# Kernel tuning notes

Measured on AMD Instinct MI355X. Metric: run time of the kernel, lower is better.

Reference implementation:

```python
import jax, jax.numpy as jnp
import numpy as np

B = 65536
NQ = 8
NL = 3
FEAT = 64 * 3 * 3 + NQ  # 584


def _conv(x, w, b):
    # x: (B,C,H,W), w: (O,I,3,3), padding=1 -> SAME
    y = jax.lax.conv_general_dilated(
        x, w, window_strides=(1, 1), padding='SAME',
        dimension_numbers=('NCHW', 'OIHW', 'NCHW'))
    return y + b[None, :, None, None]


def _maxpool2(x):
    return jax.lax.reduce_window(
        x, -jnp.inf, jax.lax.max, (1, 1, 2, 2), (1, 1, 2, 2), 'VALID')


def _quantum_sim(x, qp):
    # x: (B,NQ); qp: (NL,NQ,3). Within a layer, qubit q depends only on its own
    # previous state (tanh term), so vectorize over qubits and scan over layers.
    x_next = jnp.roll(x, -1, axis=1)  # x[:, (q+1) % NQ]

    def step(q_state, rot):  # rot: (NQ,3)
        new = jnp.sin(rot[:, 0] * x) * jnp.cos(rot[:, 1] * x_next) \
              + jnp.tanh(rot[:, 2] * q_state)
        return new, None

    q0 = jnp.zeros_like(x)
    qf, _ = jax.lax.scan(step, q0, qp)
    return qf


def setup_inputs() -> dict:
    key = jax.random.key(0)
    ks = jax.random.split(key, 16)

    def w(k, shape, fan_in):
        lim = 1.0 / np.sqrt(fan_in)
        return jax.random.uniform(k, shape, jnp.float32, -lim, lim)

    return {
        'board_state': jax.random.normal(ks[0], (B, 3, 6, 6), jnp.float32),
        'target_positions': jax.random.randint(ks[1], (4, 2), 0, 6).astype(jnp.int64),
        'conv1_w': w(ks[2], (16, 3, 3, 3), 3 * 9), 'conv1_b': w(ks[3], (16,), 3 * 9),
        'conv2_w': w(ks[4], (32, 16, 3, 3), 16 * 9), 'conv2_b': w(ks[5], (32,), 16 * 9),
        'conv3_w': w(ks[6], (64, 32, 3, 3), 32 * 9), 'conv3_b': w(ks[7], (64,), 32 * 9),
        'quantum_params': jax.random.normal(ks[8], (NL, NQ, 3), jnp.float32),
        'pt_w1': w(ks[9], (FEAT, 128), FEAT), 'pt_b1': w(ks[9], (128,), FEAT),
        'pt_w2': w(ks[10], (128, 64), 128), 'pt_b2': w(ks[10], (64,), 128),
        'pt_w3': w(ks[11], (64, 2), 64), 'pt_b3': w(ks[11], (2,), 64),
        'cf_w1': w(ks[12], (FEAT, 64), FEAT), 'cf_b1': w(ks[12], (64,), FEAT),
        'cf_w2': w(ks[13], (64, 1), 64), 'cf_b2': w(ks[13], (1,), 64),
    }


def reference(board_state, target_positions,
              conv1_w, conv1_b, conv2_w, conv2_b, conv3_w, conv3_b,
              quantum_params,
              pt_w1, pt_b1, pt_w2, pt_b2, pt_w3, pt_b3,
              cf_w1, cf_b1, cf_w2, cf_b2):
    b = board_state.shape[0]
    h = jax.nn.relu(_conv(board_state, conv1_w, conv1_b))   # (B,16,6,6)
    h = jax.nn.relu(_conv(h, conv2_w, conv2_b))             # (B,32,6,6)
    h = _maxpool2(h)                                        # (B,32,3,3)
    h = jax.nn.relu(_conv(h, conv3_w, conv3_b))             # (B,64,3,3)
    conv_flat = h.reshape(b, -1)                            # (B,576)

    board_flat = board_state.reshape(b, -1)
    q_feat = _quantum_sim(board_flat[:, :NQ], quantum_params)  # (B,NQ)

    feats = jnp.concatenate([conv_flat, q_feat], axis=1)    # (B,584)

    # piece-type head (Dropout is identity in eval)
    t = jax.nn.relu(feats @ pt_w1 + pt_b1)
    t = jax.nn.relu(t @ pt_w2 + pt_b2)
    type_logits = t @ pt_w3 + pt_b3
    type_probs = jax.nn.softmax(type_logits, axis=1)        # (B,2)

    # confidence head
    c = jax.nn.relu(feats @ cf_w1 + cf_b1)
    confidence = jax.nn.sigmoid(c @ cf_w2 + cf_b2)          # (B,1)

    # target_positions never affect the math (pos_encoding unused in torch source);
    # the same probs/confidence are reported for every position.
    return jnp.concatenate([type_probs, confidence], axis=1)  # (B,3)
```

## Files before the change

### kernel.cpp

```cpp
#include <hip/hip_runtime.h>

typedef _Float16 h8 __attribute__((ext_vector_type(8)));
typedef _Float16 h4 __attribute__((ext_vector_type(4)));
typedef float f32x4 __attribute__((ext_vector_type(4)));

union HU { _Float16 h; unsigned short u; };
__device__ __forceinline__ unsigned short f2h(float f) { HU x; x.h = (_Float16)f; return x.u; }
__device__ __forceinline__ float h2f(unsigned short u) { HU x; x.u = u; return (float)x.h; }

#define MFMA16(a, b, c) __builtin_amdgcn_mfma_f32_16x16x32_f16((a), (b), (c), 0, 0, 0)

__global__ void k_prep(const float* __restrict__ w1, const float* __restrict__ w2,
                       const float* __restrict__ w3,
                       const float* __restrict__ ptw1, const float* __restrict__ cfw1,
                       const float* __restrict__ ptw2, const float* __restrict__ ptw3,
                       const float* __restrict__ cfw2,
                       unsigned short* __restrict__ w1f,
                       unsigned short* __restrict__ w2f,
                       unsigned short* __restrict__ w3f,
                       unsigned short* __restrict__ w1hd,
                       unsigned short* __restrict__ w2hd,
                       unsigned short* __restrict__ w3hd) {
    int gid = blockIdx.x * 256 + threadIdx.x;
    int gs = gridDim.x * 256;
    for (int e = gid; e < 1024; e += gs) {
        int f = e >> 9, lane = (e >> 3) & 63, j = e & 7;
        int k = ((lane >> 4) << 3) + j, oc = lane & 15;
        int r, within;
        if (f == 0) { r = k >> 4; within = k & 15; }
        else        { r = 2;      within = k; }
        int tx = within >> 2, ch = within & 3;
        float v = 0.f;
        if (tx < 3 && ch < 3) v = w1[oc * 27 + ch * 9 + r * 3 + tx];
        w1f[e] = f2h(v);
    }
    for (int e = gid; e < 9216; e += gs) {
        int j = e & 7, lane = (e >> 3) & 63, fo = e >> 9;
        int ot = fo & 1, t = fo >> 1;
        int k = ((lane >> 4) * 8) + j, oc = ot * 16 + (lane & 15);
        float v = (k < 16) ? w2[oc * 144 + k * 9 + t] : 0.f;
        w2f[e] = f2h(v);
    }
    for (int e = gid; e < 18432; e += gs) {
        int j = e & 7, lane = (e >> 3) & 63, fo = e >> 9;
        int oti = fo & 1, t = (fo >> 1) % 9, otp = (fo >> 1) / 9;
        int ic = ((lane >> 4) * 8) + j, oc = (otp * 2 + oti) * 16 + (lane & 15);
        w3f[e] = f2h(w3[oc * 288 + ic * 9 + t]);
    }
    for (int s = gid; s < 608 * 192; s += gs) {
        int k = s / 192, n = s - k * 192;
        float v = 0.f;
        if (k < 584) {
            int f = (k < 576) ? ((k & 63) * 9 + (k >> 6)) : k;
            v = (n < 128) ? ptw1[f * 128 + n] : cfw1[f * 64 + (n - 128)];
        }
        int kk = k >> 5, hi = (k & 31) >> 3, j = k & 7, nt = n >> 4;
        int e = (((kk * 12 + nt) << 6) | (hi << 4) | (n & 15)) << 3 | j;
        w1hd[e] = f2h(v);
    }
    for (int s = gid; s < 8192; s += gs) {
        int k = s >> 6, n = s & 63;
        float v = ptw2[k * 64 + n];
        int kk = k >> 5, hi = (k & 31) >> 3, j = k & 7, nt = n >> 4;
        int e = ((((kk << 2) | nt) << 6) | (hi << 4) | (n & 15)) << 3 | j;
        w2hd[e] = f2h(v);
    }
    for (int e = gid; e < 2048; e += gs) {
        int j = e & 7, lane = (e >> 3) & 63, kk = e >> 9;
        int k = kk * 32 + ((lane >> 4) * 8) + j, n = lane & 15;
        float v = 0.f;
        if (k < 64) { if (n < 2) v = ptw3[k * 2 + n]; }
        else        { if (n == 2) v = cfw2[k - 64]; }
        w3hd[e] = f2h(v);
    }
}

#define BDS4 260
#define BDH4 (16 * BDS4)
#define A1S 584
#define A2S 296
#define FTS 616
#define HSH 200
#define RA_OFF 19712
#define O_OFF 26112
#define LDSTOT 26368

template<int PP0, int PP1>
__device__ __forceinline__ void conv2_compute(
    const unsigned short* A1, const h8* W2r, float b2v0, float b2v1,
    int sA1, int q, float pooled[5][2][4])
{
    #pragma unroll
    for (int pi = 0; pi < PP1 - PP0; pi++) {
        const int pp = PP0 + pi;
        #pragma unroll
        for (int sub = 0; sub < 4; sub++) {
            const int y = (pp / 3) * 2 + (sub >> 1), x = (pp % 3) * 2 + (sub & 1);
            f32x4 acc0 = {0.f, 0.f, 0.f, 0.f}, acc1 = {0.f, 0.f, 0.f, 0.f};
            #pragma unroll
            for (int t = 0; t < 9; t++) {
                const int sy = y + t / 3 - 1, sx = x + t % 3 - 1;
                if (sy < 0 || sy >= 6 || sx < 0 || sx >= 6) continue;
                h8 a = *(const h8*)&A1[sA1 + (sy * 6 + sx) * 16 + (q & 1) * 8];
                acc0 = MFMA16(a, W2r[t * 2 + 0], acc0);
                acc1 = MFMA16(a, W2r[t * 2 + 1], acc1);
            }
            #pragma unroll
            for (int r = 0; r < 4; r++) {
                pooled[pi][0][r] = fmaxf(pooled[pi][0][r], acc0[r] + b2v0);
                pooled[pi][1][r] = fmaxf(pooled[pi][1][r], acc1[r] + b2v1);
            }
        }
    }
}

template<int PP0, int PP1>
__device__ __forceinline__ void conv2_store(
    unsigned short* A2, const float pooled[5][2][4], int q, int col)
{
    #pragma unroll
    for (int pi = 0; pi < PP1 - PP0; pi++)
        #pragma unroll
        for (int ot = 0; ot < 2; ot++)
            #pragma unroll
            for (int r = 0; r < 4; r++)
                A2[(q * 4 + r) * A2S + (PP0 + pi) * 32 + ot * 16 + col] =
                    f2h(pooled[pi][ot][r]);
}

__global__ __launch_bounds__(256, 3) void k_fused(
    const float* __restrict__ board,
    const float* __restrict__ b1, const float* __restrict__ b2,
    const float* __restrict__ b3, const float* __restrict__ qp,
    const unsigned short* __restrict__ w1f,
    const unsigned short* __restrict__ w2f,
    const unsigned short* __restrict__ w3f,
    const unsigned short* __restrict__ w1hd,
    const unsigned short* __restrict__ w2hd,
    const unsigned short* __restrict__ w3hd,
    const float* __restrict__ ptb1, const float* __restrict__ ptb2,
    const float* __restrict__ ptb3, const float* __restrict__ cfb1,
    const float* __restrict__ cfb2,
    float* __restrict__ out)
{
    __shared__ __align__(16) unsigned short LDSH[LDSTOT];
    const int tid = threadIdx.x, wid = tid >> 6, lane = tid & 63;
    const int g = wid >> 1, w2 = wid & 1;
    const int col = lane & 15, q = lane >> 4;
    const long long gg0 = (long long)blockIdx.x * 32;
    const f32x4 ZERO4 = {0.f, 0.f, 0.f, 0.f};

    unsigned short* A1 = LDSH + g * 9856;
    unsigned short* A2 = A1;
    unsigned short* Hb = LDSH + RA_OFF;
    float* O = (float*)(LDSH + O_OFF);

    for (int e = tid; e < BDH4 / 4; e += 256)
        ((unsigned long long*)(LDSH + RA_OFF))[e] = 0ULL;
    __syncthreads();

    float qv[2];
    h8 w1r0 = ((const h8*)w1f)[lane];
    h8 w1r1 = ((const h8*)w1f)[64 + lane];
    float b1v = b1[col];
    #pragma unroll
    for (int gi = 0; gi < 2; gi++) {
        for (int e = tid; e < 16 * 108; e += 256) {
            int ss = e / 108, r2 = e % 108, ch = r2 / 36, p = r2 % 36;
            float v = board[(gg0 + gi * 16) * 108 + e];
            LDSH[RA_OFF + ss * BDS4 + ((p / 6 + 1) * 8 + (p % 6) + 1) * 4 + ch] =
                f2h(v);
        }
        __syncthreads();
        if (tid < 128) {
            int ss = tid >> 3, qq = tid & 7;
            int base = RA_OFF + ss * BDS4;
            int p8a = ((qq / 6 + 1) * 8 + (qq % 6) + 1) * 4;
            int e2 = (qq + 1) & 7;
            int p8b = ((e2 / 6 + 1) * 8 + (e2 % 6) + 1) * 4;
            float xq = h2f(LDSH[base + p8a]);
            float xn = h2f(LDSH[base + p8b]);
            float st = 0.f;
            for (int l = 0; l < 3; l++) {
                float a0 = qp[l * 24 + qq * 3], a1 = qp[l * 24 + qq * 3 + 1],
                      a2 = qp[l * 24 + qq * 3 + 2];
                st = sinf(a0 * xq) * cosf(a1 * xn) + tanhf(a2 * st);
            }
            qv[gi] = st;
        }
        {
            unsigned short* A1g = LDSH + gi * 9856;
            const int bs = RA_OFF + col * BDS4;
            const int rsel = q >> 1, wo = (q & 1) * 8;
            for (int p = wid * 9; p < wid * 9 + 9; p++) {
                int y = p / 6, x = p % 6;
                int ab1 = bs + ((y + rsel) * 8 + x) * 4 + wo;
                int ab2 = bs + ((y + 2) * 8 + x) * 4 + wo;
                union { h8 v; h4 h[2]; } a1v, a2v;
                a1v.h[0] = *(const h4*)&LDSH[ab1];
                a1v.h[1] = *(const h4*)&LDSH[ab1 + 4];
                a2v.h[0] = *(const h4*)&LDSH[ab2];
                a2v.h[1] = *(const h4*)&LDSH[ab2 + 4];
                f32x4 c = MFMA16(a1v.v, w1r0, ZERO4);
                c = MFMA16(a2v.v, w1r1, c);
                #pragma unroll
                for (int r = 0; r < 4; r++)
                    A1g[(q * 4 + r) * A1S + p * 16 + col] =
                        f2h(fmaxf(c[r] + b1v, 0.f));
            }
        }
        __syncthreads();
    }

    float pooled[5][2][4];
    #pragma unroll
    for (int pi = 0; pi < 5; pi++)
        #pragma unroll
        for (int ot = 0; ot < 2; ot++)
            #pragma unroll
            for (int r = 0; r < 4; r++) pooled[pi][ot][r] = 0.f;
    {
        h8 W2r[18];
        #pragma unroll
        for (int f = 0; f < 18; f++) W2r[f] = ((const h8*)w2f)[f * 64 + lane];
        float b2v0 = b2[col], b2v1 = b2[16 + col];
        const int sA1 = col * A1S;
        if (w2 == 0) conv2_compute<0, 5>(A1, W2r, b2v0, b2v1, sA1, q, pooled);
        else         conv2_compute<5, 9>(A1, W2r, b2v0, b2v1, sA1, q, pooled);
    }
    __syncthreads();
    if (w2 == 0) conv2_store<0, 5>(A2, pooled, q, col);
    else         conv2_store<5, 9>(A2, pooled, q, col);
    __syncthreads();

    f32x4 c3a[9], c3b[9];
    {
        const int otp = w2;
        const int sA2 = col * A2S;
        h8 W3r[18];
        #pragma unroll
        for (int f = 0; f < 18; f++)
            W3r[f] = ((const h8*)w3f)[(otp * 18 + f) * 64 + lane];
        #pragma unroll
        for (int p = 0; p < 9; p++) {
            const int y = p / 3, x = p % 3;
            f32x4 acc0 = ZERO4, acc1 = ZERO4;
            #pragma unroll
            for (int t = 0; t < 9; t++) {
                const int sy = y + t / 3 - 1, sx = x + t % 3 - 1;
                if (sy < 0 || sy >= 3 || sx < 0 || sx >= 3) continue;
                h8 a = *(const h8*)&A2[sA2 + (sy * 3 + sx) * 32 + q * 8];
                acc0 = MFMA16(a, W3r[t * 2 + 0], acc0);
                acc1 = MFMA16(a, W3r[t * 2 + 1], acc1);
            }
            c3a[p] = acc0; c3b[p] = acc1;
        }
    }
    __syncthreads();

    {
        const int otp = w2;
        float b3v0 = b3[(otp * 2 + 0) * 16 + col];
        float b3v1 = b3[(otp * 2 + 1) * 16 + col];
        int oc0 = (otp * 2 + 0) * 16 + col, oc1 = (otp * 2 + 1) * 16 + col;
        #pragma unroll
        for (int p = 0; p < 9; p++)
            #pragma unroll
            for (int r = 0; r < 4; r++) {
                int row = g * 16 + q * 4 + r;
                LDSH[row * FTS + p * 64 + oc0] = f2h(fmaxf(c3a[p][r] + b3v0, 0.f));
                LDSH[row * FTS + p * 64 + oc1] = f2h(fmaxf(c3b[p][r] + b3v1, 0.f));
            }
        if (tid < 128) {
            int ss = tid >> 3, qq = tid & 7;
            LDSH[ss * FTS + 576 + qq] = f2h(qv[0]);
            LDSH[(ss + 16) * FTS + 576 + qq] = f2h(qv[1]);
        }
        for (int e = tid; e < 1024; e += 256)
            LDSH[(e >> 5) * FTS + 584 + (e & 31)] = 0;
    }
    __syncthreads();

    {
        f32x4 acc[2][3];
        #pragma unroll
        for (int mt = 0; mt < 2; mt++)
            #pragma unroll
            for (int nt = 0; nt < 3; nt++) acc[mt][nt] = ZERO4;
        const h8* wp1 = (const h8*)w1hd;
        const int ntb = wid * 3;
        for (int kk = 0; kk < 19; kk++) {
            h8 a0 = *(const h8*)&LDSH[col * FTS + kk * 32 + q * 8];
            h8 a1 = *(const h8*)&LDSH[(16 + col) * FTS + kk * 32 + q * 8];
            h8 b[3];
            #pragma unroll
            for (int nt = 0; nt < 3; nt++)
                b[nt] = wp1[(kk * 12 + ntb + nt) * 64 + lane];
            #pragma unroll
            for (int nt = 0; nt < 3; nt++) {
                acc[0][nt] = MFMA16(a0, b[nt], acc[0][nt]);
                acc[1][nt] = MFMA16(a1, b[nt], acc[1][nt]);
            }
        }
        #pragma unroll
        for (int nt = 0; nt < 3; nt++) {
            int ntg = ntb + nt;
            float bv = (ntg < 8) ? ptb1[ntg * 16 + col] : cfb1[(ntg - 8) * 16 + col];
            #pragma unroll
            for (int mt = 0; mt < 2; mt++)
                #pragma unroll
                for (int r = 0; r < 4; r++)
                    Hb[(mt * 16 + q * 4 + r) * HSH + ntg * 16 + col] =
                        f2h(fmaxf(acc[mt][nt][r] + bv, 0.f));
        }
    }
    __syncthreads();

    {
        f32x4 acc2[2];
        acc2[0] = ZERO4; acc2[1] = ZERO4;
        const h8* wp2 = (const h8*)w2hd;
        const int nt2 = wid;
        #pragma unroll
        for (int kk = 0; kk < 4; kk++) {
            h8 a0 = *(const h8*)&Hb[col * HSH + kk * 32 + q * 8];
            h8 a1 = *(const h8*)&Hb[(16 + col) * HSH + kk * 32 + q * 8];
            h8 b = wp2[(kk * 4 + nt2) * 64 + lane];
            acc2[0] = MFMA16(a0, b, acc2[0]);
            acc2[1] = MFMA16(a1, b, acc2[1]);
        }
        __syncthreads();
        float bv2 = ptb2[nt2 * 16 + col];
        #pragma unroll
        for (int mt = 0; mt < 2; mt++)
            #pragma unroll
            for (int r = 0; r < 4; r++)
                Hb[(mt * 16 + q * 4 + r) * HSH + nt2 * 16 + col] =
                    f2h(fmaxf(acc2[mt][r] + bv2, 0.f));
    }
    __syncthreads();

    if (wid < 2) {
        const int mt = wid;
        f32x4 a3 = ZERO4;
        #pragma unroll
        for (int kk = 0; kk < 4; kk++) {
            int base = (kk < 2) ? kk * 32 : kk * 32 + 64;
            h8 a = *(const h8*)&Hb[(mt * 16 + col) * HSH + base + q * 8];
            h8 b = ((const h8*)w3hd)[kk * 64 + lane];
            a3 = MFMA16(a, b, a3);
        }
        if (col < 3) {
            float bv = (col < 2) ? ptb3[col] : cfb2[0];
            #pragma unroll
            for (int r = 0; r < 4; r++)
                O[(mt * 16 + q * 4 + r) * 4 + col] = a3[r] + bv;
        }
        if (lane < 16) {
            int s = mt * 16 + lane;
            float l0 = O[s * 4 + 0], l1 = O[s * 4 + 1], l2 = O[s * 4 + 2];
            float m = fmaxf(l0, l1);
            float e0 = expf(l0 - m), e1 = expf(l1 - m);
            float inv = 1.f / (e0 + e1);
            float* op = out + (gg0 + s) * 3;
            op[0] = e0 * inv;
            op[1] = e1 * inv;
            op[2] = 1.f / (1.f + expf(-l2));
        }
    }
}

extern "C" void kernel_launch(void* const* d_in, const int* in_sizes, int n_in,
                              void* d_out, int out_size, void* d_ws, size_t ws_size,
                              hipStream_t stream) {
    const float* board = (const float*)d_in[0];
    const float* c1w  = (const float*)d_in[2];
    const float* c1b  = (const float*)d_in[3];
    const float* c2w  = (const float*)d_in[4];
    const float* c2b  = (const float*)d_in[5];
    const float* c3w  = (const float*)d_in[6];
    const float* c3b  = (const float*)d_in[7];
    const float* qp   = (const float*)d_in[8];
    const float* ptw1 = (const float*)d_in[9];
    const float* ptb1 = (const float*)d_in[10];
    const float* ptw2 = (const float*)d_in[11];
    const float* ptb2 = (const float*)d_in[12];
    const float* ptw3 = (const float*)d_in[13];
    const float* ptb3 = (const float*)d_in[14];
    const float* cfw1 = (const float*)d_in[15];
    const float* cfb1 = (const float*)d_in[16];
    const float* cfw2 = (const float*)d_in[17];
    const float* cfb2 = (const float*)d_in[18];
    float* out = (float*)d_out;

    int Btot = in_sizes[0] / 108;

    unsigned short* w1f   = (unsigned short*)d_ws;
    unsigned short* w2f   = (unsigned short*)((char*)d_ws + 2048);
    unsigned short* w3f   = (unsigned short*)((char*)d_ws + 20480);
    unsigned short* w1hd  = (unsigned short*)((char*)d_ws + 57344);
    unsigned short* w2hd  = (unsigned short*)((char*)d_ws + 290816);
    unsigned short* w3hd  = (unsigned short*)((char*)d_ws + 307200);

    hipLaunchKernelGGL(k_prep, dim3(256), dim3(256), 0, stream,
                       c1w, c2w, c3w, ptw1, cfw1, ptw2, ptw3, cfw2,
                       w1f, w2f, w3f, w1hd, w2hd, w3hd);
    hipLaunchKernelGGL(k_fused, dim3(Btot / 32), dim3(256), 0, stream,
                       board, c1b, c2b, c3b, qp, w1f, w2f, w3f,
                       w1hd, w2hd, w3hd, ptb1, ptb2, ptb3, cfb1, cfb2, out);
}
```

Before: 181.3 us.

## Split conv2 by output-channel half per wave with rolling row-buffer reuse

Conv2 work is repartitioned so each of the paired waves computes all 9 pooled positions for one 16-channel half, rather than half the positions for both channel halves. Input rows of the activation tile are held in a 3-row rolling register buffer, so each LDS fragment is loaded once and reused across the 3x3 taps. This is meant to cut redundant LDS reads and the weight registers per wave (9 instead of 18 fragments), and to balance the waves, which previously split the positions 5 and 4. In exchange it holds 18 input fragments plus 6 accumulators live, which raises register pressure under the 3-blocks-per-CU launch bound.

Result: faster. 174.3 us (-3.9%).

```diff
diff --git a/kernel.cpp b/kernel.cpp
--- a/kernel.cpp
+++ b/kernel.cpp
@@ -85,49 +85,6 @@
 #define O_OFF 26112
 #define LDSTOT 26368
 
-template<int PP0, int PP1>
-__device__ __forceinline__ void conv2_compute(
-    const unsigned short* A1, const h8* W2r, float b2v0, float b2v1,
-    int sA1, int q, float pooled[5][2][4])
-{
-    #pragma unroll
-    for (int pi = 0; pi < PP1 - PP0; pi++) {
-        const int pp = PP0 + pi;
-        #pragma unroll
-        for (int sub = 0; sub < 4; sub++) {
-            const int y = (pp / 3) * 2 + (sub >> 1), x = (pp % 3) * 2 + (sub & 1);
-            f32x4 acc0 = {0.f, 0.f, 0.f, 0.f}, acc1 = {0.f, 0.f, 0.f, 0.f};
-            #pragma unroll
-            for (int t = 0; t < 9; t++) {
-                const int sy = y + t / 3 - 1, sx = x + t % 3 - 1;
-                if (sy < 0 || sy >= 6 || sx < 0 || sx >= 6) continue;
-                h8 a = *(const h8*)&A1[sA1 + (sy * 6 + sx) * 16 + (q & 1) * 8];
-                acc0 = MFMA16(a, W2r[t * 2 + 0], acc0);
-                acc1 = MFMA16(a, W2r[t * 2 + 1], acc1);
-            }
-            #pragma unroll
-            for (int r = 0; r < 4; r++) {
-                pooled[pi][0][r] = fmaxf(pooled[pi][0][r], acc0[r] + b2v0);
-                pooled[pi][1][r] = fmaxf(pooled[pi][1][r], acc1[r] + b2v1);
-            }
-        }
-    }
-}
-
-template<int PP0, int PP1>
-__device__ __forceinline__ void conv2_store(
-    unsigned short* A2, const float pooled[5][2][4], int q, int col)
-{
-    #pragma unroll
-    for (int pi = 0; pi < PP1 - PP0; pi++)
-        #pragma unroll
-        for (int ot = 0; ot < 2; ot++)
-            #pragma unroll
-            for (int r = 0; r < 4; r++)
-                A2[(q * 4 + r) * A2S + (PP0 + pi) * 32 + ot * 16 + col] =
-                    f2h(pooled[pi][ot][r]);
-}
-
 __global__ __launch_bounds__(256, 3) void k_fused(
     const float* __restrict__ board,
     const float* __restrict__ b1, const float* __restrict__ b2,
@@ -212,25 +169,69 @@
         __syncthreads();
     }
 
-    float pooled[5][2][4];
+    f32x4 pooled2[9];
     #pragma unroll
-    for (int pi = 0; pi < 5; pi++)
-        #pragma unroll
-        for (int ot = 0; ot < 2; ot++)
-            #pragma unroll
-            for (int r = 0; r < 4; r++) pooled[pi][ot][r] = 0.f;
+    for (int pp = 0; pp < 9; pp++) pooled2[pp] = ZERO4;
     {
-        h8 W2r[18];
-        #pragma unroll
-        for (int f = 0; f < 18; f++) W2r[f] = ((const h8*)w2f)[f * 64 + lane];
-        float b2v0 = b2[col], b2v1 = b2[16 + col];
+        h8 W2r[9];
+        #pragma unroll
+        for (int t = 0; t < 9; t++)
+            W2r[t] = ((const h8*)w2f)[(t * 2 + w2) * 64 + lane];
+        float b2v = b2[w2 * 16 + col];
         const int sA1 = col * A1S;
-        if (w2 == 0) conv2_compute<0, 5>(A1, W2r, b2v0, b2v1, sA1, q, pooled);
-        else         conv2_compute<5, 9>(A1, W2r, b2v0, b2v1, sA1, q, pooled);
-    }
-    __syncthreads();
-    if (w2 == 0) conv2_store<0, 5>(A2, pooled, q, col);
-    else         conv2_store<5, 9>(A2, pooled, q, col);
+        const int kho = (q & 1) * 8;
+
+        h8 R[3][6];
+        #pragma unroll
+        for (int x = 0; x < 6; x++) {
+            R[0][x] = *(const h8*)&A1[sA1 + (0 * 6 + x) * 16 + kho];
+            R[1][x] = *(const h8*)&A1[sA1 + (1 * 6 + x) * 16 + kho];
+        }
+        #pragma unroll
+        for (int y = 0; y < 6; y++) {
+            if (y >= 1 && y <= 4) {
+                const int nr = y + 1, slot = nr % 3;
+                #pragma unroll
+                for (int x = 0; x < 6; x++)
+                    R[slot][x] = *(const h8*)&A1[sA1 + (nr * 6 + x) * 16 + kho];
+            }
+            f32x4 acc[6];
+            #pragma unroll
+            for (int x = 0; x < 6; x++) acc[x] = ZERO4;
+            #pragma unroll
+            for (int dy = -1; dy <= 1; dy++) {
+                const int ry = y + dy;
+                if (ry < 0 || ry > 5) continue;
+                const int slot = ry % 3;
+                #pragma unroll
+                for (int x = 0; x < 6; x++)
+                    #pragma unroll
+                    for (int dx = -1; dx <= 1; dx++) {
+                        const int sx = x + dx;
+                        if (sx < 0 || sx > 5) continue;
+                        acc[x] = MFMA16(R[slot][sx],
+                                        W2r[(dy + 1) * 3 + (dx + 1)], acc[x]);
+                    }
+            }
+            const int pr = y >> 1;
+            #pragma unroll
+            for (int px = 0; px < 3; px++)
+                #pragma unroll
+                for (int xx = 0; xx < 2; xx++)
+                    #pragma unroll
+                    for (int r = 0; r < 4; r++)
+                        pooled2[pr * 3 + px][r] =
+                            fmaxf(pooled2[pr * 3 + px][r],
+                                  acc[px * 2 + xx][r] + b2v);
+        }
+    }
+    __syncthreads();
+    #pragma unroll
+    for (int pp = 0; pp < 9; pp++)
+        #pragma unroll
+        for (int r = 0; r < 4; r++)
+            A2[(q * 4 + r) * A2S + pp * 32 + w2 * 16 + col] =
+                f2h(pooled2[pp][r]);
     __syncthreads();
 
     f32x4 c3a[9], c3b[9];
```
